# Performance work log

Measured on AMD Instinct MI355X. Metric: run time of the kernel, lower is better.

The kernel has to match this reference:

```python
import jax, jax.numpy as jnp
import numpy as np

B, N, DIM = 4, 2048, 512
H, DH = 8, 64  # heads, dim_head; inner_dim = H*DH = 512
SCALE = DH ** -0.5
EPS = 1e-5


def _layer_norm(x, gamma):
    # LayerNorm with learned gamma and beta fixed to zeros (beta is a buffer)
    mu = jnp.mean(x, axis=-1, keepdims=True)
    var = jnp.var(x, axis=-1, keepdims=True)
    return (x - mu) * jax.lax.rsqrt(var + EPS) * gamma


def setup_inputs() -> dict:
    key = jax.random.key(0)
    ks = jax.random.split(key, 6)
    x = jax.random.normal(ks[0], (B, N, DIM), jnp.float32)
    mask = jax.random.bernoulli(ks[1], 0.9, (B, N))  # bool [b, n]
    gamma = jnp.ones((DIM,), jnp.float32)            # pre-attn LayerNorm gamma
    Wq = jax.random.normal(ks[2], (DIM, H * DH), jnp.float32) * 0.02
    Wkv = jax.random.normal(ks[3], (DIM, 2 * DH), jnp.float32) * 0.02  # shared single KV head (MQA)
    null_kv = jax.random.normal(ks[4], (2, DH), jnp.float32)
    Wout = jax.random.normal(ks[5], (H * DH, DIM), jnp.float32) * 0.02
    out_gamma = jnp.ones((DIM,), jnp.float32)        # post-proj LayerNorm gamma
    return {"x": x, "mask": mask, "gamma": gamma, "Wq": Wq, "Wkv": Wkv,
            "null_kv": null_kv, "Wout": Wout, "out_gamma": out_gamma}


def reference(x, mask, gamma, Wq, Wkv, null_kv, Wout, out_gamma):
    b, n, _ = x.shape
    xn = _layer_norm(x, gamma)
    # queries: per-head; keys/values: single shared head (multi-query)
    q = (xn @ Wq).reshape(b, n, H, DH).transpose(0, 2, 1, 3) * SCALE  # [b,h,n,d]
    kv = xn @ Wkv                                                     # [b,n,2d]
    k, v = kv[..., :DH], kv[..., DH:]                                 # [b,n,d]
    # prepend learned null key/value (attention sink) shared across batch
    nk = jnp.broadcast_to(null_kv[0], (b, 1, DH))
    nv = jnp.broadcast_to(null_kv[1], (b, 1, DH))
    k = jnp.concatenate([nk, k], axis=1)  # [b, n+1, d]
    v = jnp.concatenate([nv, v], axis=1)
    sim = jnp.einsum('bhid,bjd->bhij', q, k)  # [b,h,n,n+1]
    # mask padded with True for the null token, broadcast over heads/queries
    m = jnp.concatenate([jnp.ones((b, 1), bool), mask], axis=1)
    max_neg = -jnp.finfo(sim.dtype).max
    sim = jnp.where(m[:, None, None, :], sim, max_neg)
    attn = jax.nn.softmax(sim.astype(jnp.float32), axis=-1).astype(x.dtype)
    out = jnp.einsum('bhij,bjd->bhid', attn, v)       # [b,h,n,d]
    out = out.transpose(0, 2, 1, 3).reshape(b, n, H * DH)
    return _layer_norm(out @ Wout, out_gamma)
```

## Files before the change

kernel.cpp:

```cpp
#include <hip/hip_runtime.h>

typedef __attribute__((ext_vector_type(8)))  short bf16x8;
typedef __attribute__((ext_vector_type(4)))  float f32x4;
typedef __attribute__((ext_vector_type(16))) float f32x16;
typedef __attribute__((ext_vector_type(4)))  unsigned u32x4;

#define Nx 2048
#define CTXx 2049
#define KCAP 2112
#define QSCALE 0.18033688f

__device__ __forceinline__ short f2bs(float x){
    unsigned u = __builtin_bit_cast(unsigned, x);
    u = (u + 0x7fffu + ((u >> 16) & 1u)) >> 16;
    return (short)u;
}
__device__ __forceinline__ unsigned pack_trunc(float a, float b){
    return __builtin_amdgcn_perm(__builtin_bit_cast(unsigned, b),
                                 __builtin_bit_cast(unsigned, a), 0x07060302u);
}

__global__ void __launch_bounds__(256) ln1_kernel(const float* __restrict__ x,
                                                  const float* __restrict__ g,
                                                  short* __restrict__ out){
    int w = threadIdx.x >> 6, lane = threadIdx.x & 63;
    size_t row = (size_t)blockIdx.x * 4 + w;
    const float* xr = x + row * 512 + lane * 8;
    float4 a = *(const float4*)xr;
    float4 b = *(const float4*)(xr + 4);
    float s = a.x + a.y + a.z + a.w + b.x + b.y + b.z + b.w;
    float q = a.x*a.x + a.y*a.y + a.z*a.z + a.w*a.w
            + b.x*b.x + b.y*b.y + b.z*b.z + b.w*b.w;
    #pragma unroll
    for (int m = 1; m < 64; m <<= 1){ s += __shfl_xor(s, m, 64); q += __shfl_xor(q, m, 64); }
    float mu  = s * (1.f / 512.f);
    float var = fmaxf(q * (1.f / 512.f) - mu * mu, 0.f);
    float r   = rsqrtf(var + 1e-5f);
    const float* gr = g + lane * 8;
    float4 g0 = *(const float4*)gr;
    float4 g1 = *(const float4*)(gr + 4);
    bf16x8 o;
    o[0] = f2bs((a.x - mu) * r * g0.x); o[1] = f2bs((a.y - mu) * r * g0.y);
    o[2] = f2bs((a.z - mu) * r * g0.z); o[3] = f2bs((a.w - mu) * r * g0.w);
    o[4] = f2bs((b.x - mu) * r * g1.x); o[5] = f2bs((b.y - mu) * r * g1.y);
    o[6] = f2bs((b.z - mu) * r * g1.z); o[7] = f2bs((b.w - mu) * r * g1.w);
    *(bf16x8*)(out + row * 512 + lane * 8) = o;
}

__global__ void __launch_bounds__(256) ln2_kernel(const float* __restrict__ z,
                                                  const float* __restrict__ g,
                                                  float* __restrict__ out){
    int w = threadIdx.x >> 6, lane = threadIdx.x & 63;
    size_t row = (size_t)blockIdx.x * 4 + w;
    const float* xr = z + row * 512 + lane * 8;
    float4 a = *(const float4*)xr;
    float4 b = *(const float4*)(xr + 4);
    float s = a.x + a.y + a.z + a.w + b.x + b.y + b.z + b.w;
    float q = a.x*a.x + a.y*a.y + a.z*a.z + a.w*a.w
            + b.x*b.x + b.y*b.y + b.z*b.z + b.w*b.w;
    #pragma unroll
    for (int m = 1; m < 64; m <<= 1){ s += __shfl_xor(s, m, 64); q += __shfl_xor(q, m, 64); }
    float mu  = s * (1.f / 512.f);
    float var = fmaxf(q * (1.f / 512.f) - mu * mu, 0.f);
    float r   = rsqrtf(var + 1e-5f);
    const float* gr = g + lane * 8;
    float4 g0 = *(const float4*)gr;
    float4 g1 = *(const float4*)(gr + 4);
    float4 o0, o1;
    o0.x = (a.x - mu) * r * g0.x; o0.y = (a.y - mu) * r * g0.y;
    o0.z = (a.z - mu) * r * g0.z; o0.w = (a.w - mu) * r * g0.w;
    o1.x = (b.x - mu) * r * g1.x; o1.y = (b.y - mu) * r * g1.y;
    o1.z = (b.z - mu) * r * g1.z; o1.w = (b.w - mu) * r * g1.w;
    float* op = out + row * 512 + lane * 8;
    *(float4*)op = o0; *(float4*)(op + 4) = o1;
}

__global__ void __launch_bounds__(256) prep_kernel(const float* __restrict__ Wq,
                                                   const float* __restrict__ Wkv,
                                                   const float* __restrict__ Wout,
                                                   const float* __restrict__ nkv,
                                                   short* __restrict__ WcatT,
                                                   short* __restrict__ WoutT,
                                                   short* __restrict__ kb,
                                                   short* __restrict__ vbt){
    int bid = blockIdx.x, t = threadIdx.x;
    if (bid == 144){
        int b = t >> 6, d = t & 63;
        kb[((size_t)b * KCAP) * 64 + d] = f2bs(nkv[d]);
        vbt[((size_t)b * 64 + d) * KCAP + 0] = f2bs(nkv[64 + d]);
        return;
    }
    __shared__ float ls[64][65];
    bool isOut = (bid >= 80);
    int b2 = isOut ? bid - 80 : bid;
    int ntile = isOut ? (b2 & 7) : (b2 % 10);
    int ktile = isOut ? (b2 >> 3) : (b2 / 10);
    int n0 = ntile * 64, k0 = ktile * 64;
    #pragma unroll
    for (int rr = 0; rr < 64; rr += 16){
        int r = rr + (t >> 4), c = (t & 15) * 4;
        float4 v;
        if (isOut)            v = *(const float4*)(Wout + (size_t)(k0 + r) * 512 + n0 + c);
        else if (n0 < 512)    v = *(const float4*)(Wq   + (size_t)(k0 + r) * 512 + n0 + c);
        else                  v = *(const float4*)(Wkv  + (size_t)(k0 + r) * 128 + (n0 - 512) + c);
        ls[c + 0][r] = v.x; ls[c + 1][r] = v.y; ls[c + 2][r] = v.z; ls[c + 3][r] = v.w;
    }
    __syncthreads();
    int rn = t >> 2, kc = (t & 3) * 16;
    short tmp[16];
    #pragma unroll
    for (int j = 0; j < 16; j++) tmp[j] = f2bs(ls[rn][kc + j]);
    short* dst = (isOut ? WoutT : WcatT) + (size_t)(n0 + rn) * 512 + k0 + kc;
    *(int4*)dst       = *(int4*)&tmp[0];
    *(int4*)(dst + 8) = *(int4*)&tmp[8];
}

template<int MODE>
__global__ void __launch_bounds__(256, 2) gemm_mfma(const short* __restrict__ A,
                                                    const short* __restrict__ BwT,
                                                    short* __restrict__ qb,
                                                    short* __restrict__ kb,
                                                    short* __restrict__ vbt,
                                                    float* __restrict__ C){
    __shared__ short As[2][128][72];
    __shared__ short Bs[2][128][72];
    int t = threadIdx.x;
    int lane = t & 63, w = t >> 6;
    int l16 = lane & 15, quad = lane >> 4;
    int wm = w & 1, wn = w >> 1;
    int row0 = blockIdx.y * 128, col0 = blockIdx.x * 128;
    f32x4 acc[4][4];
    #pragma unroll
    for (int i = 0; i < 4; i++)
        #pragma unroll
        for (int j = 0; j < 4; j++) acc[i][j] = (f32x4){0.f, 0.f, 0.f, 0.f};
    int ar = t >> 1, ak = (t & 1) * 32;
    const short* ap = A   + (size_t)(row0 + ar) * 512 + ak;
    const short* bp = BwT + (size_t)(col0 + ar) * 512 + ak;
    int4 a0 = *(const int4*)(ap);      int4 a1 = *(const int4*)(ap + 8);
    int4 a2 = *(const int4*)(ap + 16); int4 a3 = *(const int4*)(ap + 24);
    int4 b0 = *(const int4*)(bp);      int4 b1 = *(const int4*)(bp + 8);
    int4 b2 = *(const int4*)(bp + 16); int4 b3 = *(const int4*)(bp + 24);
    int p = 0;
    for (int k0 = 0; k0 < 512; k0 += 64){
        *(int4*)&As[p][ar][ak]      = a0;
        *(int4*)&As[p][ar][ak + 8]  = a1;
        *(int4*)&As[p][ar][ak + 16] = a2;
        *(int4*)&As[p][ar][ak + 24] = a3;
        *(int4*)&Bs[p][ar][ak]      = b0;
        *(int4*)&Bs[p][ar][ak + 8]  = b1;
        *(int4*)&Bs[p][ar][ak + 16] = b2;
        *(int4*)&Bs[p][ar][ak + 24] = b3;
        __syncthreads();
        int kn = k0 + 64;
        if (kn < 512){
            a0 = *(const int4*)(ap + kn);      a1 = *(const int4*)(ap + kn + 8);
            a2 = *(const int4*)(ap + kn + 16); a3 = *(const int4*)(ap + kn + 24);
            b0 = *(const int4*)(bp + kn);      b1 = *(const int4*)(bp + kn + 8);
            b2 = *(const int4*)(bp + kn + 16); b3 = *(const int4*)(bp + kn + 24);
        }
        #pragma unroll
        for (int ks = 0; ks < 2; ks++){
            bf16x8 af[4], bfr[4];
            #pragma unroll
            for (int mt = 0; mt < 4; mt++)
                af[mt] = *(const bf16x8*)&As[p][wm * 64 + mt * 16 + l16][ks * 32 + quad * 8];
            #pragma unroll
            for (int nt = 0; nt < 4; nt++)
                bfr[nt] = *(const bf16x8*)&Bs[p][wn * 64 + nt * 16 + l16][ks * 32 + quad * 8];
            #pragma unroll
            for (int mt = 0; mt < 4; mt++)
                #pragma unroll
                for (int nt = 0; nt < 4; nt++)
                    acc[mt][nt] = __builtin_amdgcn_mfma_f32_16x16x32_bf16(af[mt], bfr[nt], acc[mt][nt], 0, 0, 0);
        }
        p ^= 1;
    }
    #pragma unroll
    for (int mt = 0; mt < 4; mt++)
        #pragma unroll
        for (int nt = 0; nt < 4; nt++)
            #pragma unroll
            for (int r = 0; r < 4; r++){
                int row = row0 + wm * 64 + mt * 16 + quad * 4 + r;
                int col = col0 + wn * 64 + nt * 16 + l16;
                float v = acc[mt][nt][r];
                if (MODE == 0){
                    int bb = row >> 11, ii = row & 2047;
                    if (col < 512){
                        qb[(size_t)row * 512 + col] = f2bs(v * QSCALE);
                    } else if (col < 576){
                        kb[((size_t)bb * KCAP + ii + 1) * 64 + (col - 512)] = f2bs(v);
                    } else {
                        vbt[((size_t)bb * 64 + (col - 576)) * KCAP + ii + 1] = f2bs(v);
                    }
                } else {
                    C[(size_t)row * 512 + col] = v;
                }
            }
}

__global__ void __launch_bounds__(256, 2) attn_kernel(const short* __restrict__ qb,
                                                      const short* __restrict__ kb,
                                                      const short* __restrict__ vbt,
                                                      const int* __restrict__ mask,
                                                      short* __restrict__ ob){
    __shared__ short Vt[2][64][72];
    int t = threadIdx.x;
    int lane = t & 63, w = t >> 6;
    int n32 = lane & 31, hb = lane >> 5;
    int b = blockIdx.y, i0 = blockIdx.x * 16;
    int head = 2 * w + (n32 >> 4), row = i0 + (n32 & 15);
    bf16x8 qf[4];
    {
        const short* qp = qb + ((size_t)(b * Nx + row)) * 512 + head * 64 + hb * 8;
        #pragma unroll
        for (int ks = 0; ks < 4; ks++) qf[ks] = *(const bf16x8*)(qp + ks * 16);
    }
    bf16x8 ones;
    #pragma unroll
    for (int j = 0; j < 8; j++) ones[j] = (short)0x3F80;
    f32x16 oacc[2], lacc;
    #pragma unroll
    for (int j = 0; j < 16; j++){ oacc[0][j] = 0.f; oacc[1][j] = 0.f; lacc[j] = 0.f; }

    int vd = t >> 2, vk = (t & 3) * 16;
    const short* vgp = vbt + ((size_t)b * 64 + vd) * KCAP + vk;
    const short* kfb = kb  + (size_t)b * KCAP * 64 + (size_t)n32 * 64 + hb * 8;
    const int* mrow = mask + b * Nx;

    int4 pv0 = *(const int4*)(vgp);
    int4 pv1 = *(const int4*)(vgp + 8);
    bf16x8 kfr[2][4];
    #pragma unroll
    for (int ks = 0; ks < 4; ks++){
        kfr[0][ks] = *(const bf16x8*)(kfb + ks * 16);
        kfr[1][ks] = *(const bf16x8*)(kfb + 2048 + ks * 16);
    }
    int mok = (lane == 0) ? 1 : ((lane < CTXx) ? mrow[lane - 1] : 0);

    int p = 0;
    for (int j0 = 0; j0 < KCAP; j0 += 64){
        *(int4*)&Vt[p][vd][vk]     = make_int4(pv0.x, pv0.y, pv1.x, pv1.y);
        *(int4*)&Vt[p][vd][vk + 8] = make_int4(pv0.z, pv0.w, pv1.z, pv1.w);
        __syncthreads();
        unsigned long long bal = __ballot(mok != 0);
        f32x16 sf[2];
        #pragma unroll
        for (int i = 0; i < 2; i++)
            #pragma unroll
            for (int j = 0; j < 16; j++) sf[i][j] = 0.f;
        #pragma unroll
        for (int ks = 0; ks < 4; ks++){
            sf[0] = __builtin_amdgcn_mfma_f32_32x32x16_bf16(kfr[0][ks], qf[ks], sf[0], 0, 0, 0);
            sf[1] = __builtin_amdgcn_mfma_f32_32x32x16_bf16(kfr[1][ks], qf[ks], sf[1], 0, 0, 0);
        }
        int jn = j0 + 64;
        if (jn < KCAP){
            pv0 = *(const int4*)(vgp + jn);
            pv1 = *(const int4*)(vgp + jn + 8);
            const short* kp = kfb + (size_t)jn * 64;
            #pragma unroll
            for (int ks = 0; ks < 4; ks++){
                kfr[0][ks] = *(const bf16x8*)(kp + ks * 16);
                kfr[1][ks] = *(const bf16x8*)(kp + 2048 + ks * 16);
            }
            int jg = jn + lane;
            mok = (jg < CTXx) ? mrow[jg - 1] : 0;
        }
        unsigned mlo = (unsigned)(bal >> (4 * hb));
        unsigned mhi = (unsigned)(bal >> (32 + 4 * hb));
        unsigned pg[8][2];
        #pragma unroll
        for (int kt = 0; kt < 2; kt++){
            unsigned mm = kt ? mhi : mlo;
            #pragma unroll
            for (int g4 = 0; g4 < 4; g4++){
                float pr[4];
                #pragma unroll
                for (int tt = 0; tt < 4; tt++){
                    float e = __builtin_amdgcn_exp2f(sf[kt][g4 * 4 + tt]);
                    pr[tt] = ((mm >> (8 * g4 + tt)) & 1u) ? e : 0.f;
                }
                pg[kt * 4 + g4][0] = pack_trunc(pr[0], pr[1]);
                pg[kt * 4 + g4][1] = pack_trunc(pr[2], pr[3]);
            }
        }
        #pragma unroll
        for (int s = 0; s < 4; s++){
            bf16x8 pa = __builtin_bit_cast(bf16x8,
                (u32x4){pg[2 * s][0], pg[2 * s][1], pg[2 * s + 1][0], pg[2 * s + 1][1]});
            lacc = __builtin_amdgcn_mfma_f32_32x32x16_bf16(pa, ones, lacc, 0, 0, 0);
            #pragma unroll
            for (int nt = 0; nt < 2; nt++){
                bf16x8 vf = *(const bf16x8*)&Vt[p][nt * 32 + n32][s * 16 + hb * 8];
                oacc[nt] = __builtin_amdgcn_mfma_f32_32x32x16_bf16(pa, vf, oacc[nt], 0, 0, 0);
            }
        }
        p ^= 1;
    }
    #pragma unroll
    for (int r = 0; r < 16; r++){
        float linv = 1.f / lacc[r];
        int hr = (r & 3) + 8 * (r >> 2) + 4 * hb;
        int grow = i0 + (hr & 15);
        int ghead = 2 * w + (hr >> 4);
        short* op = ob + ((size_t)(b * Nx + grow)) * 512 + ghead * 64 + n32;
        op[0]  = f2bs(oacc[0][r] * linv);
        op[32] = f2bs(oacc[1][r] * linv);
    }
}

extern "C" void kernel_launch(void* const* d_in, const int* in_sizes, int n_in,
                              void* d_out, int out_size, void* d_ws, size_t ws_size,
                              hipStream_t stream){
    const float* x     = (const float*)d_in[0];
    const int*   mask  = (const int*)  d_in[1];
    const float* gamma = (const float*)d_in[2];
    const float* Wq    = (const float*)d_in[3];
    const float* Wkv   = (const float*)d_in[4];
    const float* nkv   = (const float*)d_in[5];
    const float* Wout  = (const float*)d_in[6];
    const float* og    = (const float*)d_in[7];
    float* out = (float*)d_out;

    short* xnb   = (short*)d_ws;
    short* qb    = xnb + (size_t)4194304;
    short* kb    = qb  + (size_t)4194304;
    short* vbt   = kb  + (size_t)540672;
    short* ob    = vbt + (size_t)540672;
    short* WcatT = ob  + (size_t)4194304;
    short* WoutT = WcatT + (size_t)327680;
    float* zb    = (float*)d_ws;

    ln1_kernel  <<<2048, 256, 0, stream>>>(x, gamma, xnb);
    prep_kernel <<<145, 256, 0, stream>>>(Wq, Wkv, Wout, nkv, WcatT, WoutT, kb, vbt);
    gemm_mfma<0><<<dim3(5, 64), 256, 0, stream>>>(xnb, WcatT, qb, kb, vbt, nullptr);
    attn_kernel <<<dim3(128, 4), 256, 0, stream>>>(qb, kb, vbt, mask, ob);
    gemm_mfma<1><<<dim3(4, 64), 256, 0, stream>>>(ob, WoutT, nullptr, nullptr, nullptr, zb);
    ln2_kernel  <<<2048, 256, 0, stream>>>(zb, og, out);
}
```

Before: 192.9 us.

## Split attention over key range, stage K in LDS, fuse LN1 with weight prep

The attention kernel's key range is split into two halves along a new grid z dimension, which doubles the block count from 512 to 1024. Each half writes unnormalized partial outputs and row sums, and a new reduce kernel combines them and normalizes. K tiles are now staged through shared memory instead of being loaded per lane into registers, and launch bounds allow 4 blocks per CU. LN1 and weight preparation are merged into one launch. The cost is an extra bf16 round trip and an extra kernel for the split reduction. This works without a running-max rescale only because the softmax skips max subtraction, so the partial sums add directly.

```diff
diff --git a/kernel.cpp b/kernel.cpp
--- a/kernel.cpp
+++ b/kernel.cpp
@@ -15,36 +15,81 @@
     u = (u + 0x7fffu + ((u >> 16) & 1u)) >> 16;
     return (short)u;
 }
+__device__ __forceinline__ float us2f(unsigned short u){
+    union { unsigned i; float f; } c; c.i = ((unsigned)u) << 16; return c.f;
+}
 __device__ __forceinline__ unsigned pack_trunc(float a, float b){
     return __builtin_amdgcn_perm(__builtin_bit_cast(unsigned, b),
                                  __builtin_bit_cast(unsigned, a), 0x07060302u);
 }
 
-__global__ void __launch_bounds__(256) ln1_kernel(const float* __restrict__ x,
-                                                  const float* __restrict__ g,
-                                                  short* __restrict__ out){
-    int w = threadIdx.x >> 6, lane = threadIdx.x & 63;
-    size_t row = (size_t)blockIdx.x * 4 + w;
-    const float* xr = x + row * 512 + lane * 8;
-    float4 a = *(const float4*)xr;
-    float4 b = *(const float4*)(xr + 4);
-    float s = a.x + a.y + a.z + a.w + b.x + b.y + b.z + b.w;
-    float q = a.x*a.x + a.y*a.y + a.z*a.z + a.w*a.w
-            + b.x*b.x + b.y*b.y + b.z*b.z + b.w*b.w;
-    #pragma unroll
-    for (int m = 1; m < 64; m <<= 1){ s += __shfl_xor(s, m, 64); q += __shfl_xor(q, m, 64); }
-    float mu  = s * (1.f / 512.f);
-    float var = fmaxf(q * (1.f / 512.f) - mu * mu, 0.f);
-    float r   = rsqrtf(var + 1e-5f);
-    const float* gr = g + lane * 8;
-    float4 g0 = *(const float4*)gr;
-    float4 g1 = *(const float4*)(gr + 4);
-    bf16x8 o;
-    o[0] = f2bs((a.x - mu) * r * g0.x); o[1] = f2bs((a.y - mu) * r * g0.y);
-    o[2] = f2bs((a.z - mu) * r * g0.z); o[3] = f2bs((a.w - mu) * r * g0.w);
-    o[4] = f2bs((b.x - mu) * r * g1.x); o[5] = f2bs((b.y - mu) * r * g1.y);
-    o[6] = f2bs((b.z - mu) * r * g1.z); o[7] = f2bs((b.w - mu) * r * g1.w);
-    *(bf16x8*)(out + row * 512 + lane * 8) = o;
+__global__ void __launch_bounds__(256) ln1_prep_kernel(const float* __restrict__ x,
+                                                       const float* __restrict__ g,
+                                                       short* __restrict__ xnb,
+                                                       const float* __restrict__ Wq,
+                                                       const float* __restrict__ Wkv,
+                                                       const float* __restrict__ Wout,
+                                                       const float* __restrict__ nkv,
+                                                       short* __restrict__ WcatT,
+                                                       short* __restrict__ WoutT,
+                                                       short* __restrict__ kb,
+                                                       short* __restrict__ vbt){
+    __shared__ float ls[64][65];
+    int t = threadIdx.x;
+    if (blockIdx.x < 2048){
+        int w = t >> 6, lane = t & 63;
+        size_t row = (size_t)blockIdx.x * 4 + w;
+        const float* xr = x + row * 512 + lane * 8;
+        float4 a = *(const float4*)xr;
+        float4 b = *(const float4*)(xr + 4);
+        float s = a.x + a.y + a.z + a.w + b.x + b.y + b.z + b.w;
+        float q = a.x*a.x + a.y*a.y + a.z*a.z + a.w*a.w
+                + b.x*b.x + b.y*b.y + b.z*b.z + b.w*b.w;
+        #pragma unroll
+        for (int m = 1; m < 64; m <<= 1){ s += __shfl_xor(s, m, 64); q += __shfl_xor(q, m, 64); }
+        float mu  = s * (1.f / 512.f);
+        float var = fmaxf(q * (1.f / 512.f) - mu * mu, 0.f);
+        float r   = rsqrtf(var + 1e-5f);
+        const float* gr = g + lane * 8;
+        float4 g0 = *(const float4*)gr;
+        float4 g1 = *(const float4*)(gr + 4);
+        bf16x8 o;
+        o[0] = f2bs((a.x - mu) * r * g0.x); o[1] = f2bs((a.y - mu) * r * g0.y);
+        o[2] = f2bs((a.z - mu) * r * g0.z); o[3] = f2bs((a.w - mu) * r * g0.w);
+        o[4] = f2bs((b.x - mu) * r * g1.x); o[5] = f2bs((b.y - mu) * r * g1.y);
+        o[6] = f2bs((b.z - mu) * r * g1.z); o[7] = f2bs((b.w - mu) * r * g1.w);
+        *(bf16x8*)(xnb + row * 512 + lane * 8) = o;
+        return;
+    }
+    int bid = blockIdx.x - 2048;
+    if (bid == 144){
+        int b = t >> 6, d = t & 63;
+        kb[((size_t)b * KCAP) * 64 + d] = f2bs(nkv[d]);
+        vbt[((size_t)b * 64 + d) * KCAP + 0] = f2bs(nkv[64 + d]);
+        return;
+    }
+    bool isOut = (bid >= 80);
+    int b2 = isOut ? bid - 80 : bid;
+    int ntile = isOut ? (b2 & 7) : (b2 % 10);
+    int ktile = isOut ? (b2 >> 3) : (b2 / 10);
+    int n0 = ntile * 64, k0 = ktile * 64;
+    #pragma unroll
+    for (int rr = 0; rr < 64; rr += 16){
+        int r = rr + (t >> 4), c = (t & 15) * 4;
+        float4 v;
+        if (isOut)            v = *(const float4*)(Wout + (size_t)(k0 + r) * 512 + n0 + c);
+        else if (n0 < 512)    v = *(const float4*)(Wq   + (size_t)(k0 + r) * 512 + n0 + c);
+        else                  v = *(const float4*)(Wkv  + (size_t)(k0 + r) * 128 + (n0 - 512) + c);
+        ls[c + 0][r] = v.x; ls[c + 1][r] = v.y; ls[c + 2][r] = v.z; ls[c + 3][r] = v.w;
+    }
+    __syncthreads();
+    int rn = t >> 2, kc = (t & 3) * 16;
+    short tmp[16];
+    #pragma unroll
+    for (int j = 0; j < 16; j++) tmp[j] = f2bs(ls[rn][kc + j]);
+    short* dst = (isOut ? WoutT : WcatT) + (size_t)(n0 + rn) * 512 + k0 + kc;
+    *(int4*)dst       = *(int4*)&tmp[0];
+    *(int4*)(dst + 8) = *(int4*)&tmp[8];
 }
 
 __global__ void __launch_bounds__(256) ln2_kernel(const float* __restrict__ z,
@@ -73,46 +118,6 @@
     o1.z = (b.z - mu) * r * g1.z; o1.w = (b.w - mu) * r * g1.w;
     float* op = out + row * 512 + lane * 8;
     *(float4*)op = o0; *(float4*)(op + 4) = o1;
-}
-
-__global__ void __launch_bounds__(256) prep_kernel(const float* __restrict__ Wq,
-                                                   const float* __restrict__ Wkv,
-                                                   const float* __restrict__ Wout,
-                                                   const float* __restrict__ nkv,
-                                                   short* __restrict__ WcatT,
-                                                   short* __restrict__ WoutT,
-                                                   short* __restrict__ kb,
-                                                   short* __restrict__ vbt){
-    int bid = blockIdx.x, t = threadIdx.x;
-    if (bid == 144){
-        int b = t >> 6, d = t & 63;
-        kb[((size_t)b * KCAP) * 64 + d] = f2bs(nkv[d]);
-        vbt[((size_t)b * 64 + d) * KCAP + 0] = f2bs(nkv[64 + d]);
-        return;
-    }
-    __shared__ float ls[64][65];
-    bool isOut = (bid >= 80);
-    int b2 = isOut ? bid - 80 : bid;
-    int ntile = isOut ? (b2 & 7) : (b2 % 10);
-    int ktile = isOut ? (b2 >> 3) : (b2 / 10);
-    int n0 = ntile * 64, k0 = ktile * 64;
-    #pragma unroll
-    for (int rr = 0; rr < 64; rr += 16){
-        int r = rr + (t >> 4), c = (t & 15) * 4;
-        float4 v;
-        if (isOut)            v = *(const float4*)(Wout + (size_t)(k0 + r) * 512 + n0 + c);
-        else if (n0 < 512)    v = *(const float4*)(Wq   + (size_t)(k0 + r) * 512 + n0 + c);
-        else                  v = *(const float4*)(Wkv  + (size_t)(k0 + r) * 128 + (n0 - 512) + c);
-        ls[c + 0][r] = v.x; ls[c + 1][r] = v.y; ls[c + 2][r] = v.z; ls[c + 3][r] = v.w;
-    }
-    __syncthreads();
-    int rn = t >> 2, kc = (t & 3) * 16;
-    short tmp[16];
-    #pragma unroll
-    for (int j = 0; j < 16; j++) tmp[j] = f2bs(ls[rn][kc + j]);
-    short* dst = (isOut ? WoutT : WcatT) + (size_t)(n0 + rn) * 512 + k0 + kc;
-    *(int4*)dst       = *(int4*)&tmp[0];
-    *(int4*)(dst + 8) = *(int4*)&tmp[8];
 }
 
 template<int MODE>
@@ -200,16 +205,19 @@
             }
 }
 
-__global__ void __launch_bounds__(256, 2) attn_kernel(const short* __restrict__ qb,
+__global__ void __launch_bounds__(256, 4) attn_kernel(const short* __restrict__ qb,
                                                       const short* __restrict__ kb,
                                                       const short* __restrict__ vbt,
                                                       const int* __restrict__ mask,
-                                                      short* __restrict__ ob){
+                                                      short* __restrict__ obp,
+                                                      float* __restrict__ lp){
+    __shared__ short Ks[2][64][72];
     __shared__ short Vt[2][64][72];
     int t = threadIdx.x;
     int lane = t & 63, w = t >> 6;
     int n32 = lane & 31, hb = lane >> 5;
-    int b = blockIdx.y, i0 = blockIdx.x * 16;
+    int b = blockIdx.y, i0 = blockIdx.x * 16, half = blockIdx.z;
+    int jt0 = half ? 17 : 0, jt1 = half ? 33 : 17;
     int head = 2 * w + (n32 >> 4), row = i0 + (n32 & 15);
     bf16x8 qf[4];
     {
@@ -224,49 +232,49 @@
     #pragma unroll
     for (int j = 0; j < 16; j++){ oacc[0][j] = 0.f; oacc[1][j] = 0.f; lacc[j] = 0.f; }
 
-    int vd = t >> 2, vk = (t & 3) * 16;
+    int skey = t >> 2, sd = (t & 3) * 16;
+    int vd   = t >> 2, vk = (t & 3) * 16;
+    const short* kgp = kb  + (size_t)b * KCAP * 64 + skey * 64 + sd;
     const short* vgp = vbt + ((size_t)b * 64 + vd) * KCAP + vk;
-    const short* kfb = kb  + (size_t)b * KCAP * 64 + (size_t)n32 * 64 + hb * 8;
     const int* mrow = mask + b * Nx;
 
-    int4 pv0 = *(const int4*)(vgp);
-    int4 pv1 = *(const int4*)(vgp + 8);
-    bf16x8 kfr[2][4];
-    #pragma unroll
-    for (int ks = 0; ks < 4; ks++){
-        kfr[0][ks] = *(const bf16x8*)(kfb + ks * 16);
-        kfr[1][ks] = *(const bf16x8*)(kfb + 2048 + ks * 16);
-    }
-    int mok = (lane == 0) ? 1 : ((lane < CTXx) ? mrow[lane - 1] : 0);
+    int j0 = jt0 * 64;
+    int4 pk0 = *(const int4*)(kgp + (size_t)j0 * 64);
+    int4 pk1 = *(const int4*)(kgp + (size_t)j0 * 64 + 8);
+    int4 pv0 = *(const int4*)(vgp + j0);
+    int4 pv1 = *(const int4*)(vgp + j0 + 8);
+    int jg0 = j0 + lane;
+    int mok = (jg0 == 0) ? 1 : ((jg0 < CTXx) ? mrow[jg0 - 1] : 0);
 
     int p = 0;
-    for (int j0 = 0; j0 < KCAP; j0 += 64){
-        *(int4*)&Vt[p][vd][vk]     = make_int4(pv0.x, pv0.y, pv1.x, pv1.y);
-        *(int4*)&Vt[p][vd][vk + 8] = make_int4(pv0.z, pv0.w, pv1.z, pv1.w);
+    for (int jt = jt0; jt < jt1; ++jt){
+        *(int4*)&Ks[p][skey][sd]     = pk0;
+        *(int4*)&Ks[p][skey][sd + 8] = pk1;
+        *(int4*)&Vt[p][vd][vk]       = make_int4(pv0.x, pv0.y, pv1.x, pv1.y);
+        *(int4*)&Vt[p][vd][vk + 8]   = make_int4(pv0.z, pv0.w, pv1.z, pv1.w);
+        unsigned long long bal = __ballot(mok != 0);
         __syncthreads();
-        unsigned long long bal = __ballot(mok != 0);
-        f32x16 sf[2];
-        #pragma unroll
-        for (int i = 0; i < 2; i++)
-            #pragma unroll
-            for (int j = 0; j < 16; j++) sf[i][j] = 0.f;
-        #pragma unroll
-        for (int ks = 0; ks < 4; ks++){
-            sf[0] = __builtin_amdgcn_mfma_f32_32x32x16_bf16(kfr[0][ks], qf[ks], sf[0], 0, 0, 0);
-            sf[1] = __builtin_amdgcn_mfma_f32_32x32x16_bf16(kfr[1][ks], qf[ks], sf[1], 0, 0, 0);
-        }
-        int jn = j0 + 64;
-        if (jn < KCAP){
+        int jn = (jt + 1) * 64;
+        if (jt + 1 < jt1){
+            pk0 = *(const int4*)(kgp + (size_t)jn * 64);
+            pk1 = *(const int4*)(kgp + (size_t)jn * 64 + 8);
             pv0 = *(const int4*)(vgp + jn);
             pv1 = *(const int4*)(vgp + jn + 8);
-            const short* kp = kfb + (size_t)jn * 64;
-            #pragma unroll
-            for (int ks = 0; ks < 4; ks++){
-                kfr[0][ks] = *(const bf16x8*)(kp + ks * 16);
-                kfr[1][ks] = *(const bf16x8*)(kp + 2048 + ks * 16);
-            }
             int jg = jn + lane;
             mok = (jg < CTXx) ? mrow[jg - 1] : 0;
+        }
+        f32x16 sf[2];
+        #pragma unroll
+        for (int i = 0; i < 2; i++)
+            #pragma unroll
+            for (int j = 0; j < 16; j++) sf[i][j] = 0.f;
+        #pragma unroll
+        for (int ks = 0; ks < 4; ks++){
+            #pragma unroll
+            for (int kt = 0; kt < 2; kt++){
+                bf16x8 kf = *(const bf16x8*)&Ks[p][kt * 32 + n32][ks * 16 + hb * 8];
+                sf[kt] = __builtin_amdgcn_mfma_f32_32x32x16_bf16(kf, qf[ks], sf[kt], 0, 0, 0);
+            }
         }
         unsigned mlo = (unsigned)(bal >> (4 * hb));
         unsigned mhi = (unsigned)(bal >> (32 + 4 * hb));
@@ -299,16 +307,35 @@
         }
         p ^= 1;
     }
+    short* opb = obp + (size_t)half * 8192 * 512;
+    float* lpb = lp  + (size_t)half * 65536;
     #pragma unroll
     for (int r = 0; r < 16; r++){
-        float linv = 1.f / lacc[r];
         int hr = (r & 3) + 8 * (r >> 2) + 4 * hb;
         int grow = i0 + (hr & 15);
         int ghead = 2 * w + (hr >> 4);
-        short* op = ob + ((size_t)(b * Nx + grow)) * 512 + ghead * 64 + n32;
-        op[0]  = f2bs(oacc[0][r] * linv);
-        op[32] = f2bs(oacc[1][r] * linv);
-    }
+        short* op = opb + ((size_t)(b * Nx + grow)) * 512 + ghead * 64 + n32;
+        op[0]  = f2bs(oacc[0][r]);
+        op[32] = f2bs(oacc[1][r]);
+        if (n32 == 0) lpb[(size_t)(b * Nx + grow) * 8 + ghead] = lacc[r];
+    }
+}
+
+__global__ void __launch_bounds__(256) reduce_kernel(const short* __restrict__ obp,
+                                                     const float* __restrict__ lp,
+                                                     short* __restrict__ ob){
+    int rowg = blockIdx.x;
+    int t = threadIdx.x;
+    int c = t * 2;
+    int head = c >> 6;
+    float L = lp[(size_t)rowg * 8 + head] + lp[65536 + (size_t)rowg * 8 + head];
+    float linv = 1.f / L;
+    unsigned u0 = *(const unsigned*)(obp + (size_t)rowg * 512 + c);
+    unsigned u1 = *(const unsigned*)(obp + (size_t)8192 * 512 + (size_t)rowg * 512 + c);
+    float o0 = (us2f((unsigned short)u0) + us2f((unsigned short)u1)) * linv;
+    float o1 = (us2f((unsigned short)(u0 >> 16)) + us2f((unsigned short)(u1 >> 16))) * linv;
+    unsigned packed = ((unsigned)(unsigned short)f2bs(o1) << 16) | (unsigned)(unsigned short)f2bs(o0);
+    *(unsigned*)(ob + (size_t)rowg * 512 + c) = packed;
 }
 
 extern "C" void kernel_launch(void* const* d_in, const int* in_sizes, int n_in,
@@ -325,18 +352,22 @@
     float* out = (float*)d_out;
 
     short* xnb   = (short*)d_ws;
-    short* qb    = xnb + (size_t)4194304;
-    short* kb    = qb  + (size_t)4194304;
-    short* vbt   = kb  + (size_t)540672;
-    short* ob    = vbt + (size_t)540672;
-    short* WcatT = ob  + (size_t)4194304;
+    short* obp1  = xnb  + (size_t)4194304;
+    short* qb    = obp1 + (size_t)4194304;
+    short* kb    = qb   + (size_t)4194304;
+    short* vbt   = kb   + (size_t)540672;
+    short* WcatT = vbt  + (size_t)540672;
     short* WoutT = WcatT + (size_t)327680;
+    float* Lp    = (float*)(WoutT + 262144);
+    short* obp   = xnb;
+    short* ob    = qb;
     float* zb    = (float*)d_ws;
 
-    ln1_kernel  <<<2048, 256, 0, stream>>>(x, gamma, xnb);
-    prep_kernel <<<145, 256, 0, stream>>>(Wq, Wkv, Wout, nkv, WcatT, WoutT, kb, vbt);
-    gemm_mfma<0><<<dim3(5, 64), 256, 0, stream>>>(xnb, WcatT, qb, kb, vbt, nullptr);
-    attn_kernel <<<dim3(128, 4), 256, 0, stream>>>(qb, kb, vbt, mask, ob);
-    gemm_mfma<1><<<dim3(4, 64), 256, 0, stream>>>(ob, WoutT, nullptr, nullptr, nullptr, zb);
-    ln2_kernel  <<<2048, 256, 0, stream>>>(zb, og, out);
-}
+    ln1_prep_kernel<<<2193, 256, 0, stream>>>(x, gamma, xnb, Wq, Wkv, Wout, nkv,
+                                              WcatT, WoutT, kb, vbt);
+    gemm_mfma<0>  <<<dim3(5, 64), 256, 0, stream>>>(xnb, WcatT, qb, kb, vbt, nullptr);
+    attn_kernel   <<<dim3(128, 4, 2), 256, 0, stream>>>(qb, kb, vbt, mask, obp, Lp);
+    reduce_kernel <<<8192, 256, 0, stream>>>(obp, Lp, ob);
+    gemm_mfma<1>  <<<dim3(4, 64), 256, 0, stream>>>(ob, WoutT, nullptr, nullptr, nullptr, zb);
+    ln2_kernel    <<<2048, 256, 0, stream>>>(zb, og, out);
+}
```

New measurement: 233.8 us. 21.2% more time.

## Fuse LN1 with weight prep, widen QKV GEMM tiles, stage K through LDS

Applied to the files above, without the earlier changes.

Merges the LayerNorm and weight-transpose kernels into one launch, which removes one launch. The QKV GEMM now uses 128x160 tiles, so a grid of 4x64 covers all 640 columns and the odd fifth column of blocks goes away, at the cost of more registers and occupancy pinned at 1. The attention kernel now loads each 64-key K tile cooperatively into LDS and double-buffers it, instead of each wave fetching K fragments from global memory. This cuts redundant global loads but adds LDS traffic and shared memory.

```diff
diff --git a/kernel.cpp b/kernel.cpp
--- a/kernel.cpp
+++ b/kernel.cpp
@@ -20,31 +20,73 @@
                                  __builtin_bit_cast(unsigned, a), 0x07060302u);
 }
 
-__global__ void __launch_bounds__(256) ln1_kernel(const float* __restrict__ x,
-                                                  const float* __restrict__ g,
-                                                  short* __restrict__ out){
-    int w = threadIdx.x >> 6, lane = threadIdx.x & 63;
-    size_t row = (size_t)blockIdx.x * 4 + w;
-    const float* xr = x + row * 512 + lane * 8;
-    float4 a = *(const float4*)xr;
-    float4 b = *(const float4*)(xr + 4);
-    float s = a.x + a.y + a.z + a.w + b.x + b.y + b.z + b.w;
-    float q = a.x*a.x + a.y*a.y + a.z*a.z + a.w*a.w
-            + b.x*b.x + b.y*b.y + b.z*b.z + b.w*b.w;
-    #pragma unroll
-    for (int m = 1; m < 64; m <<= 1){ s += __shfl_xor(s, m, 64); q += __shfl_xor(q, m, 64); }
-    float mu  = s * (1.f / 512.f);
-    float var = fmaxf(q * (1.f / 512.f) - mu * mu, 0.f);
-    float r   = rsqrtf(var + 1e-5f);
-    const float* gr = g + lane * 8;
-    float4 g0 = *(const float4*)gr;
-    float4 g1 = *(const float4*)(gr + 4);
-    bf16x8 o;
-    o[0] = f2bs((a.x - mu) * r * g0.x); o[1] = f2bs((a.y - mu) * r * g0.y);
-    o[2] = f2bs((a.z - mu) * r * g0.z); o[3] = f2bs((a.w - mu) * r * g0.w);
-    o[4] = f2bs((b.x - mu) * r * g1.x); o[5] = f2bs((b.y - mu) * r * g1.y);
-    o[6] = f2bs((b.z - mu) * r * g1.z); o[7] = f2bs((b.w - mu) * r * g1.w);
-    *(bf16x8*)(out + row * 512 + lane * 8) = o;
+__global__ void __launch_bounds__(256) ln1_prep_kernel(const float* __restrict__ x,
+                                                       const float* __restrict__ g,
+                                                       short* __restrict__ xnb,
+                                                       const float* __restrict__ Wq,
+                                                       const float* __restrict__ Wkv,
+                                                       const float* __restrict__ Wout,
+                                                       const float* __restrict__ nkv,
+                                                       short* __restrict__ WcatT,
+                                                       short* __restrict__ WoutT,
+                                                       short* __restrict__ kb,
+                                                       short* __restrict__ vbt){
+    __shared__ float ls[64][65];
+    int t = threadIdx.x;
+    if (blockIdx.x < 2048){
+        int w = t >> 6, lane = t & 63;
+        size_t row = (size_t)blockIdx.x * 4 + w;
+        const float* xr = x + row * 512 + lane * 8;
+        float4 a = *(const float4*)xr;
+        float4 b = *(const float4*)(xr + 4);
+        float s = a.x + a.y + a.z + a.w + b.x + b.y + b.z + b.w;
+        float q = a.x*a.x + a.y*a.y + a.z*a.z + a.w*a.w
+                + b.x*b.x + b.y*b.y + b.z*b.z + b.w*b.w;
+        #pragma unroll
+        for (int m = 1; m < 64; m <<= 1){ s += __shfl_xor(s, m, 64); q += __shfl_xor(q, m, 64); }
+        float mu  = s * (1.f / 512.f);
+        float var = fmaxf(q * (1.f / 512.f) - mu * mu, 0.f);
+        float r   = rsqrtf(var + 1e-5f);
+        const float* gr = g + lane * 8;
+        float4 g0 = *(const float4*)gr;
+        float4 g1 = *(const float4*)(gr + 4);
+        bf16x8 o;
+        o[0] = f2bs((a.x - mu) * r * g0.x); o[1] = f2bs((a.y - mu) * r * g0.y);
+        o[2] = f2bs((a.z - mu) * r * g0.z); o[3] = f2bs((a.w - mu) * r * g0.w);
+        o[4] = f2bs((b.x - mu) * r * g1.x); o[5] = f2bs((b.y - mu) * r * g1.y);
+        o[6] = f2bs((b.z - mu) * r * g1.z); o[7] = f2bs((b.w - mu) * r * g1.w);
+        *(bf16x8*)(xnb + row * 512 + lane * 8) = o;
+        return;
+    }
+    int bid = blockIdx.x - 2048;
+    if (bid == 144){
+        int b = t >> 6, d = t & 63;
+        kb[((size_t)b * KCAP) * 64 + d] = f2bs(nkv[d]);
+        vbt[((size_t)b * 64 + d) * KCAP + 0] = f2bs(nkv[64 + d]);
+        return;
+    }
+    bool isOut = (bid >= 80);
+    int b2 = isOut ? bid - 80 : bid;
+    int ntile = isOut ? (b2 & 7) : (b2 % 10);
+    int ktile = isOut ? (b2 >> 3) : (b2 / 10);
+    int n0 = ntile * 64, k0 = ktile * 64;
+    #pragma unroll
+    for (int rr = 0; rr < 64; rr += 16){
+        int r = rr + (t >> 4), c = (t & 15) * 4;
+        float4 v;
+        if (isOut)            v = *(const float4*)(Wout + (size_t)(k0 + r) * 512 + n0 + c);
+        else if (n0 < 512)    v = *(const float4*)(Wq   + (size_t)(k0 + r) * 512 + n0 + c);
+        else                  v = *(const float4*)(Wkv  + (size_t)(k0 + r) * 128 + (n0 - 512) + c);
+        ls[c + 0][r] = v.x; ls[c + 1][r] = v.y; ls[c + 2][r] = v.z; ls[c + 3][r] = v.w;
+    }
+    __syncthreads();
+    int rn = t >> 2, kc = (t & 3) * 16;
+    short tmp[16];
+    #pragma unroll
+    for (int j = 0; j < 16; j++) tmp[j] = f2bs(ls[rn][kc + j]);
+    short* dst = (isOut ? WoutT : WcatT) + (size_t)(n0 + rn) * 512 + k0 + kc;
+    *(int4*)dst       = *(int4*)&tmp[0];
+    *(int4*)(dst + 8) = *(int4*)&tmp[8];
 }
 
 __global__ void __launch_bounds__(256) ln2_kernel(const float* __restrict__ z,
@@ -75,53 +117,93 @@
     *(float4*)op = o0; *(float4*)(op + 4) = o1;
 }
 
-__global__ void __launch_bounds__(256) prep_kernel(const float* __restrict__ Wq,
-                                                   const float* __restrict__ Wkv,
-                                                   const float* __restrict__ Wout,
-                                                   const float* __restrict__ nkv,
-                                                   short* __restrict__ WcatT,
-                                                   short* __restrict__ WoutT,
+__global__ void __launch_bounds__(256, 1) gemm_qkv(const short* __restrict__ A,
+                                                   const short* __restrict__ BwT,
+                                                   short* __restrict__ qb,
                                                    short* __restrict__ kb,
                                                    short* __restrict__ vbt){
-    int bid = blockIdx.x, t = threadIdx.x;
-    if (bid == 144){
-        int b = t >> 6, d = t & 63;
-        kb[((size_t)b * KCAP) * 64 + d] = f2bs(nkv[d]);
-        vbt[((size_t)b * 64 + d) * KCAP + 0] = f2bs(nkv[64 + d]);
-        return;
-    }
-    __shared__ float ls[64][65];
-    bool isOut = (bid >= 80);
-    int b2 = isOut ? bid - 80 : bid;
-    int ntile = isOut ? (b2 & 7) : (b2 % 10);
-    int ktile = isOut ? (b2 >> 3) : (b2 / 10);
-    int n0 = ntile * 64, k0 = ktile * 64;
-    #pragma unroll
-    for (int rr = 0; rr < 64; rr += 16){
-        int r = rr + (t >> 4), c = (t & 15) * 4;
-        float4 v;
-        if (isOut)            v = *(const float4*)(Wout + (size_t)(k0 + r) * 512 + n0 + c);
-        else if (n0 < 512)    v = *(const float4*)(Wq   + (size_t)(k0 + r) * 512 + n0 + c);
-        else                  v = *(const float4*)(Wkv  + (size_t)(k0 + r) * 128 + (n0 - 512) + c);
-        ls[c + 0][r] = v.x; ls[c + 1][r] = v.y; ls[c + 2][r] = v.z; ls[c + 3][r] = v.w;
-    }
-    __syncthreads();
-    int rn = t >> 2, kc = (t & 3) * 16;
-    short tmp[16];
-    #pragma unroll
-    for (int j = 0; j < 16; j++) tmp[j] = f2bs(ls[rn][kc + j]);
-    short* dst = (isOut ? WoutT : WcatT) + (size_t)(n0 + rn) * 512 + k0 + kc;
-    *(int4*)dst       = *(int4*)&tmp[0];
-    *(int4*)(dst + 8) = *(int4*)&tmp[8];
-}
-
-template<int MODE>
-__global__ void __launch_bounds__(256, 2) gemm_mfma(const short* __restrict__ A,
-                                                    const short* __restrict__ BwT,
-                                                    short* __restrict__ qb,
-                                                    short* __restrict__ kb,
-                                                    short* __restrict__ vbt,
-                                                    float* __restrict__ C){
+    __shared__ short As[2][128][72];
+    __shared__ short Bs[2][160][72];
+    int t = threadIdx.x;
+    int lane = t & 63, w = t >> 6;
+    int l16 = lane & 15, quad = lane >> 4;
+    int wm = w & 1, wn = w >> 1;
+    int row0 = blockIdx.y * 128, col0 = blockIdx.x * 160;
+    f32x4 acc[4][5];
+    #pragma unroll
+    for (int i = 0; i < 4; i++)
+        #pragma unroll
+        for (int j = 0; j < 5; j++) acc[i][j] = (f32x4){0.f, 0.f, 0.f, 0.f};
+    int ar = t >> 1, ak = (t & 1) * 32;
+    const short* ap = A + (size_t)(row0 + ar) * 512 + ak;
+    int4 a0 = *(const int4*)(ap);      int4 a1 = *(const int4*)(ap + 8);
+    int4 a2 = *(const int4*)(ap + 16); int4 a3 = *(const int4*)(ap + 24);
+    int4 pb[5];
+    int brow[5], bseg[5];
+    #pragma unroll
+    for (int ps = 0; ps < 5; ps++){
+        int idx = ps * 256 + t;
+        brow[ps] = idx >> 3; bseg[ps] = (idx & 7) * 8;
+        pb[ps] = *(const int4*)(BwT + (size_t)(col0 + brow[ps]) * 512 + bseg[ps]);
+    }
+    int p = 0;
+    for (int k0 = 0; k0 < 512; k0 += 64){
+        *(int4*)&As[p][ar][ak]      = a0;
+        *(int4*)&As[p][ar][ak + 8]  = a1;
+        *(int4*)&As[p][ar][ak + 16] = a2;
+        *(int4*)&As[p][ar][ak + 24] = a3;
+        #pragma unroll
+        for (int ps = 0; ps < 5; ps++)
+            *(int4*)&Bs[p][brow[ps]][bseg[ps]] = pb[ps];
+        __syncthreads();
+        int kn = k0 + 64;
+        if (kn < 512){
+            a0 = *(const int4*)(ap + kn);      a1 = *(const int4*)(ap + kn + 8);
+            a2 = *(const int4*)(ap + kn + 16); a3 = *(const int4*)(ap + kn + 24);
+            #pragma unroll
+            for (int ps = 0; ps < 5; ps++)
+                pb[ps] = *(const int4*)(BwT + (size_t)(col0 + brow[ps]) * 512 + kn + bseg[ps]);
+        }
+        #pragma unroll
+        for (int ks = 0; ks < 2; ks++){
+            bf16x8 af[4], bfr[5];
+            #pragma unroll
+            for (int mt = 0; mt < 4; mt++)
+                af[mt] = *(const bf16x8*)&As[p][wm * 64 + mt * 16 + l16][ks * 32 + quad * 8];
+            #pragma unroll
+            for (int nt = 0; nt < 5; nt++)
+                bfr[nt] = *(const bf16x8*)&Bs[p][wn * 80 + nt * 16 + l16][ks * 32 + quad * 8];
+            #pragma unroll
+            for (int mt = 0; mt < 4; mt++)
+                #pragma unroll
+                for (int nt = 0; nt < 5; nt++)
+                    acc[mt][nt] = __builtin_amdgcn_mfma_f32_16x16x32_bf16(af[mt], bfr[nt], acc[mt][nt], 0, 0, 0);
+        }
+        p ^= 1;
+    }
+    #pragma unroll
+    for (int mt = 0; mt < 4; mt++)
+        #pragma unroll
+        for (int nt = 0; nt < 5; nt++)
+            #pragma unroll
+            for (int r = 0; r < 4; r++){
+                int row = row0 + wm * 64 + mt * 16 + quad * 4 + r;
+                int col = col0 + wn * 80 + nt * 16 + l16;
+                float v = acc[mt][nt][r];
+                int bb = row >> 11, ii = row & 2047;
+                if (col < 512){
+                    qb[(size_t)row * 512 + col] = f2bs(v * QSCALE);
+                } else if (col < 576){
+                    kb[((size_t)bb * KCAP + ii + 1) * 64 + (col - 512)] = f2bs(v);
+                } else {
+                    vbt[((size_t)bb * 64 + (col - 576)) * KCAP + ii + 1] = f2bs(v);
+                }
+            }
+}
+
+__global__ void __launch_bounds__(256, 2) gemm_out(const short* __restrict__ A,
+                                                   const short* __restrict__ BwT,
+                                                   float* __restrict__ C){
     __shared__ short As[2][128][72];
     __shared__ short Bs[2][128][72];
     int t = threadIdx.x;
@@ -184,19 +266,7 @@
             for (int r = 0; r < 4; r++){
                 int row = row0 + wm * 64 + mt * 16 + quad * 4 + r;
                 int col = col0 + wn * 64 + nt * 16 + l16;
-                float v = acc[mt][nt][r];
-                if (MODE == 0){
-                    int bb = row >> 11, ii = row & 2047;
-                    if (col < 512){
-                        qb[(size_t)row * 512 + col] = f2bs(v * QSCALE);
-                    } else if (col < 576){
-                        kb[((size_t)bb * KCAP + ii + 1) * 64 + (col - 512)] = f2bs(v);
-                    } else {
-                        vbt[((size_t)bb * 64 + (col - 576)) * KCAP + ii + 1] = f2bs(v);
-                    }
-                } else {
-                    C[(size_t)row * 512 + col] = v;
-                }
+                C[(size_t)row * 512 + col] = acc[mt][nt][r];
             }
 }
 
@@ -205,6 +275,7 @@
                                                       const short* __restrict__ vbt,
                                                       const int* __restrict__ mask,
                                                       short* __restrict__ ob){
+    __shared__ short Ks[2][64][72];
     __shared__ short Vt[2][64][72];
     int t = threadIdx.x;
     int lane = t & 63, w = t >> 6;
@@ -224,49 +295,47 @@
     #pragma unroll
     for (int j = 0; j < 16; j++){ oacc[0][j] = 0.f; oacc[1][j] = 0.f; lacc[j] = 0.f; }
 
-    int vd = t >> 2, vk = (t & 3) * 16;
+    int skey = t >> 2, sd = (t & 3) * 16;
+    int vd   = t >> 2, vk = (t & 3) * 16;
+    const short* kgp = kb  + (size_t)b * KCAP * 64 + skey * 64 + sd;
     const short* vgp = vbt + ((size_t)b * 64 + vd) * KCAP + vk;
-    const short* kfb = kb  + (size_t)b * KCAP * 64 + (size_t)n32 * 64 + hb * 8;
     const int* mrow = mask + b * Nx;
 
+    int4 pk0 = *(const int4*)(kgp);
+    int4 pk1 = *(const int4*)(kgp + 8);
     int4 pv0 = *(const int4*)(vgp);
     int4 pv1 = *(const int4*)(vgp + 8);
-    bf16x8 kfr[2][4];
-    #pragma unroll
-    for (int ks = 0; ks < 4; ks++){
-        kfr[0][ks] = *(const bf16x8*)(kfb + ks * 16);
-        kfr[1][ks] = *(const bf16x8*)(kfb + 2048 + ks * 16);
-    }
     int mok = (lane == 0) ? 1 : ((lane < CTXx) ? mrow[lane - 1] : 0);
 
     int p = 0;
-    for (int j0 = 0; j0 < KCAP; j0 += 64){
-        *(int4*)&Vt[p][vd][vk]     = make_int4(pv0.x, pv0.y, pv1.x, pv1.y);
-        *(int4*)&Vt[p][vd][vk + 8] = make_int4(pv0.z, pv0.w, pv1.z, pv1.w);
+    for (int jt = 0; jt < 33; ++jt){
+        *(int4*)&Ks[p][skey][sd]     = pk0;
+        *(int4*)&Ks[p][skey][sd + 8] = pk1;
+        *(int4*)&Vt[p][vd][vk]       = make_int4(pv0.x, pv0.y, pv1.x, pv1.y);
+        *(int4*)&Vt[p][vd][vk + 8]   = make_int4(pv0.z, pv0.w, pv1.z, pv1.w);
+        unsigned long long bal = __ballot(mok != 0);
         __syncthreads();
-        unsigned long long bal = __ballot(mok != 0);
-        f32x16 sf[2];
-        #pragma unroll
-        for (int i = 0; i < 2; i++)
-            #pragma unroll
-            for (int j = 0; j < 16; j++) sf[i][j] = 0.f;
-        #pragma unroll
-        for (int ks = 0; ks < 4; ks++){
-            sf[0] = __builtin_amdgcn_mfma_f32_32x32x16_bf16(kfr[0][ks], qf[ks], sf[0], 0, 0, 0);
-            sf[1] = __builtin_amdgcn_mfma_f32_32x32x16_bf16(kfr[1][ks], qf[ks], sf[1], 0, 0, 0);
-        }
-        int jn = j0 + 64;
-        if (jn < KCAP){
+        int jn = (jt + 1) * 64;
+        if (jt + 1 < 33){
+            pk0 = *(const int4*)(kgp + (size_t)jn * 64);
+            pk1 = *(const int4*)(kgp + (size_t)jn * 64 + 8);
             pv0 = *(const int4*)(vgp + jn);
             pv1 = *(const int4*)(vgp + jn + 8);
-            const short* kp = kfb + (size_t)jn * 64;
-            #pragma unroll
-            for (int ks = 0; ks < 4; ks++){
-                kfr[0][ks] = *(const bf16x8*)(kp + ks * 16);
-                kfr[1][ks] = *(const bf16x8*)(kp + 2048 + ks * 16);
-            }
             int jg = jn + lane;
             mok = (jg < CTXx) ? mrow[jg - 1] : 0;
+        }
+        f32x16 sf[2];
+        #pragma unroll
+        for (int i = 0; i < 2; i++)
+            #pragma unroll
+            for (int j = 0; j < 16; j++) sf[i][j] = 0.f;
+        #pragma unroll
+        for (int ks = 0; ks < 4; ks++){
+            #pragma unroll
+            for (int kt = 0; kt < 2; kt++){
+                bf16x8 kf = *(const bf16x8*)&Ks[p][kt * 32 + n32][ks * 16 + hb * 8];
+                sf[kt] = __builtin_amdgcn_mfma_f32_32x32x16_bf16(kf, qf[ks], sf[kt], 0, 0, 0);
+            }
         }
         unsigned mlo = (unsigned)(bal >> (4 * hb));
         unsigned mhi = (unsigned)(bal >> (32 + 4 * hb));
@@ -333,10 +402,10 @@
     short* WoutT = WcatT + (size_t)327680;
     float* zb    = (float*)d_ws;
 
-    ln1_kernel  <<<2048, 256, 0, stream>>>(x, gamma, xnb);
-    prep_kernel <<<145, 256, 0, stream>>>(Wq, Wkv, Wout, nkv, WcatT, WoutT, kb, vbt);
-    gemm_mfma<0><<<dim3(5, 64), 256, 0, stream>>>(xnb, WcatT, qb, kb, vbt, nullptr);
+    ln1_prep_kernel<<<2193, 256, 0, stream>>>(x, gamma, xnb, Wq, Wkv, Wout, nkv,
+                                              WcatT, WoutT, kb, vbt);
+    gemm_qkv    <<<dim3(4, 64), 256, 0, stream>>>(xnb, WcatT, qb, kb, vbt);
     attn_kernel <<<dim3(128, 4), 256, 0, stream>>>(qb, kb, vbt, mask, ob);
-    gemm_mfma<1><<<dim3(4, 64), 256, 0, stream>>>(ob, WoutT, nullptr, nullptr, nullptr, zb);
+    gemm_out    <<<dim3(4, 64), 256, 0, stream>>>(ob, WoutT, zb);
     ln2_kernel  <<<2048, 256, 0, stream>>>(zb, og, out);
 }
```

Measured after the change: 180.2 us. -6.5%, faster.
